# Kernel optimization log

Hardware: AMD Instinct MI355X
Metric: run time of the kernel (lower is better)

## Reference

```python
import jax, jax.numpy as jnp
import numpy as np

D_MODEL = 768
NUM_HEADS = 12
D_K = D_MODEL // NUM_HEADS


def setup_inputs() -> dict:
    key = jax.random.key(0)
    ks = jax.random.split(key, 12)
    B, S = 4, 2048
    s = 1.0 / np.sqrt(D_MODEL)
    inp = {
        "query": jax.random.normal(ks[0], (B, S, D_MODEL), jnp.float32),
        "key": jax.random.normal(ks[1], (B, S, D_MODEL), jnp.float32),
        "value": jax.random.normal(ks[2], (B, S, D_MODEL), jnp.float32),
        "Wq": jax.random.normal(ks[3], (D_MODEL, D_MODEL), jnp.float32) * s,
        "bq": jnp.zeros((D_MODEL,), jnp.float32),
        "Wk": jax.random.normal(ks[4], (D_MODEL, D_MODEL), jnp.float32) * s,
        "bk": jnp.zeros((D_MODEL,), jnp.float32),
        "Wv": jax.random.normal(ks[5], (D_MODEL, D_MODEL), jnp.float32) * s,
        "bv": jnp.zeros((D_MODEL,), jnp.float32),
        "Wo": jax.random.normal(ks[6], (D_MODEL, D_MODEL), jnp.float32) * s,
        "bo": jnp.zeros((D_MODEL,), jnp.float32),
    }
    return inp


def _split_heads(x):
    B, S, _ = x.shape
    return x.reshape(B, S, NUM_HEADS, D_K).transpose(0, 2, 1, 3)  # [B,H,S,Dk]


def reference(query, key, value, Wq, bq, Wk, bk, Wv, bv, Wo, bo):
    # Linear projections (torch nn.Linear: x @ W.T + b)
    Q = _split_heads(query @ Wq.T + bq)
    K = _split_heads(key @ Wk.T + bk)
    V = _split_heads(value @ Wv.T + bv)
    scale = 1.0 / jnp.sqrt(jnp.asarray(D_K, Q.dtype))
    scores = jnp.einsum("bhqd,bhkd->bhqk", Q, K) * scale  # [B,H,S,S]
    attn = jax.nn.softmax(scores, axis=-1)
    # dropout is identity in eval mode
    out = jnp.einsum("bhqk,bhkd->bhqd", attn, V)  # [B,H,S,Dk]
    B, H, S, Dk = out.shape
    out = out.transpose(0, 2, 1, 3).reshape(B, S, H * Dk)
    return out @ Wo.T + bo
```

## Files before the change

kernel.cpp:

```cpp
#include <hip/hip_runtime.h>
#include <hip/hip_bf16.h>

typedef _Float16 half8 __attribute__((ext_vector_type(8)));
typedef _Float16 h4 __attribute__((ext_vector_type(4)));
typedef __fp16 fp16x2 __attribute__((ext_vector_type(2)));
typedef float f32x4 __attribute__((ext_vector_type(4)));

#define D_MODEL 768
#define NUM_HEADS 12
#define D_K 64
#define SEQ 2048
#define BATCH 4
#define M_TOTAL (BATCH * SEQ)
#define W_ELEMS (D_MODEL * D_MODEL)
#define X_ELEMS (M_TOTAL * D_MODEL)
#define QSCALE 0.18033688011112042f
#define SOFF 4.0f

__device__ __forceinline__ void gll16(const _Float16* g, _Float16* l) {
    __builtin_amdgcn_global_load_lds(
        (const __attribute__((address_space(1))) unsigned int*)g,
        (__attribute__((address_space(3))) unsigned int*)l,
        16, 0, 0);
}

__global__ void convert_all(
    const float* __restrict__ w0, const float* __restrict__ w1,
    const float* __restrict__ w2, const float* __restrict__ w3,
    const float* __restrict__ x0, const float* __restrict__ x1,
    const float* __restrict__ x2, _Float16* __restrict__ dst)
{
    const size_t W4 = W_ELEMS / 4, X4 = X_ELEMS / 4;
    size_t i = (size_t)blockIdx.x * blockDim.x + threadIdx.x;
    const float* src;
    size_t off;
    if (i < 4 * W4) {
        size_t slab = i / W4;
        off = i - slab * W4;
        src = (slab == 0) ? w0 : (slab == 1) ? w1 : (slab == 2) ? w2 : w3;
    } else {
        size_t j = i - 4 * W4;
        size_t slab = j / X4;
        off = j - slab * X4;
        src = (slab == 0) ? x0 : (slab == 1) ? x1 : x2;
    }
    float4 f = ((const float4*)src)[off];
    h4 h;
    h[0] = (_Float16)f.x; h[1] = (_Float16)f.y;
    h[2] = (_Float16)f.z; h[3] = (_Float16)f.w;
    ((h4*)dst)[i] = h;
}

__global__ __launch_bounds__(256) void gemm_qkv(
    const _Float16* __restrict__ Xall, const _Float16* __restrict__ Wall,
    const float* __restrict__ bq, const float* __restrict__ bk, const float* __restrict__ bv,
    _Float16* __restrict__ Qo, _Float16* __restrict__ Ko, _Float16* __restrict__ Vto)
{
    __shared__ __align__(16) char smem[36864];
    _Float16* As = (_Float16*)smem;
    _Float16* Bs = As + 128 * 64;

    const int z = blockIdx.z;
    const _Float16* X = Xall + (size_t)z * X_ELEMS;
    const _Float16* W = Wall + (size_t)z * W_ELEMS;

    const int t = threadIdx.x;
    const int w = t >> 6;
    const int l = t & 63;
    const int ln = t & 15;
    const int quad = (t >> 4) & 3;
    const int wm = w >> 1, wn = w & 1;
    const int m0 = blockIdx.x * 128, n0 = blockIdx.y * 128;

    const int srow = l >> 3;
    const int scol = (l & 7) ^ srow;

    f32x4 acc[4][4] = {};

    for (int k0 = 0; k0 < D_MODEL; k0 += 64) {
#pragma unroll
        for (int jj = 0; jj < 4; ++jj) {
            int j = w * 4 + jj;
            int row = j * 8 + srow;
            gll16(X + (size_t)(m0 + row) * D_MODEL + k0 + scol * 8, As + j * 512);
            gll16(W + (size_t)(n0 + row) * D_MODEL + k0 + scol * 8, Bs + j * 512);
        }
        __syncthreads();

#pragma unroll
        for (int kk = 0; kk < 2; ++kk) {
            half8 a[4], b[4];
#pragma unroll
            for (int i = 0; i < 4; ++i) {
                int ra = wm * 64 + i * 16 + ln;
                int rb = wn * 64 + i * 16 + ln;
                a[i] = *(const half8*)&As[ra * 64 + (((kk * 4 + quad) ^ (ln & 7)) * 8)];
                b[i] = *(const half8*)&Bs[rb * 64 + (((kk * 4 + quad) ^ (ln & 7)) * 8)];
            }
            if (z <= 1) {
#pragma unroll
                for (int i = 0; i < 4; ++i)
#pragma unroll
                    for (int j2 = 0; j2 < 4; ++j2)
                        acc[i][j2] = __builtin_amdgcn_mfma_f32_16x16x32_f16(b[j2], a[i], acc[i][j2], 0, 0, 0);
            } else {
#pragma unroll
                for (int i = 0; i < 4; ++i)
#pragma unroll
                    for (int j2 = 0; j2 < 4; ++j2)
                        acc[i][j2] = __builtin_amdgcn_mfma_f32_16x16x32_f16(a[i], b[j2], acc[i][j2], 0, 0, 0);
            }
        }
        __syncthreads();
    }

    if (z <= 1) {
        const float* bias = (z == 0) ? bq : bk;
        _Float16* dst = (z == 0) ? Qo : Ko;
        const int head = (n0 + wn * 64) >> 6;
#pragma unroll
        for (int i = 0; i < 4; ++i) {
            int m = m0 + wm * 64 + i * 16 + ln;
            int b_ = m >> 11, s_ = m & 2047;
            _Float16* rowp = dst + ((size_t)((b_ * NUM_HEADS + head) * SEQ + s_)) * D_K;
#pragma unroll
            for (int j = 0; j < 4; ++j) {
                int dbase = j * 16 + quad * 4;
                f32x4 bn = *(const f32x4*)&bias[n0 + wn * 64 + dbase];
                h4 o;
#pragma unroll
                for (int r = 0; r < 4; ++r) {
                    float v = acc[i][j][r] + bn[r];
                    if (z == 0) v *= QSCALE;
                    o[r] = (_Float16)v;
                }
                *(h4*)&rowp[dbase] = o;
            }
        }
    } else {
        const float* bias = bv;
        _Float16* T = (_Float16*)smem + (size_t)w * (64 * 72);
#pragma unroll
        for (int i = 0; i < 4; ++i) {
#pragma unroll
            for (int j = 0; j < 4; ++j) {
                float bn = bias[n0 + wn * 64 + j * 16 + ln];
                h4 hh;
#pragma unroll
                for (int r = 0; r < 4; ++r) hh[r] = (_Float16)(acc[i][j][r] + bn);
                *(h4*)&T[(j * 16 + ln) * 72 + i * 16 + quad * 4] = hh;
            }
        }
        const int b_ = m0 >> 11;
        const int s0 = (m0 & 2047) + wm * 64;
        const int head = (n0 >> 6) + wn;
        _Float16* base = Vto + (size_t)(b_ * NUM_HEADS + head) * D_K * SEQ + s0;
        const int p = l & 7, tt = p >> 2, qq = p & 3;
#pragma unroll
        for (int r8 = 0; r8 < 8; ++r8) {
            int nl = r8 * 8 + (l >> 3);
            h4 lo = *(const h4*)&T[nl * 72 + tt * 32 + qq * 4];
            h4 hi = *(const h4*)&T[nl * 72 + tt * 32 + 16 + qq * 4];
            half8 v = __builtin_shufflevector(lo, hi, 0, 1, 2, 3, 4, 5, 6, 7);
            *(half8*)(base + (size_t)nl * SEQ + p * 8) = v;
        }
    }
}

__global__ __launch_bounds__(512, 6) void attn(
    const _Float16* __restrict__ Qg, const _Float16* __restrict__ Kg,
    const _Float16* __restrict__ Vtg, _Float16* __restrict__ ctx)
{
    __shared__ __align__(16) _Float16 Ks[2][64 * 64];
    __shared__ __align__(16) _Float16 Vs[2][64 * 64];

    const int t = threadIdx.x;
    const int w = t >> 6;
    const int l = t & 63;
    const int ln = t & 15;
    const int quad = (t >> 4) & 3;

    const int lid = blockIdx.x + (int)gridDim.x * blockIdx.y;
    const int nid = (lid & 7) * ((SEQ / 128) * (BATCH * NUM_HEADS) / 8) + (lid >> 3);
    const int bh = nid >> 4;
    const int q0 = (nid & 15) * 128 + w * 16;

    const _Float16* Qh = Qg + (size_t)bh * SEQ * D_K;
    const _Float16* Kh = Kg + (size_t)bh * SEQ * D_K;
    const _Float16* Vh = Vtg + (size_t)bh * D_K * SEQ;

    const int srow = l >> 3;
    const int scol = (l & 7) ^ srow;
    const _Float16* Ksrc = Kh + (size_t)(w * 8 + srow) * D_K + scol * 8;
    const _Float16* Vsrc = Vh + (size_t)(w * 8 + srow) * SEQ + scol * 8;

    half8 qf[2];
#pragma unroll
    for (int dh = 0; dh < 2; ++dh)
        qf[dh] = *(const half8*)(Qh + (size_t)(q0 + ln) * D_K + dh * 32 + quad * 8);

    f32x4 acc[4] = {};
    f32x4 lsum = {};

    gll16(Ksrc, &Ks[0][w * 512]);
    gll16(Vsrc, &Vs[0][w * 512]);
    asm volatile("s_waitcnt vmcnt(0)" ::: "memory");
    __builtin_amdgcn_s_barrier();

    int cur = 0;
    for (int c = 0; c < SEQ / 64; ++c) {
        if (c + 1 < SEQ / 64) {
            gll16(Ksrc + (size_t)(c + 1) * 64 * D_K, &Ks[cur ^ 1][w * 512]);
            gll16(Vsrc + (size_t)(c + 1) * 64, &Vs[cur ^ 1][w * 512]);
        }

        const _Float16* Ksc = Ks[cur];
        const _Float16* Vsc = Vs[cur];

        h4 pB[4];
#pragma unroll
        for (int kt = 0; kt < 4; ++kt) {
            half8 kf0 = *(const half8*)&Ksc[(kt * 16 + ln) * 64 + ((quad ^ (ln & 7)) * 8)];
            half8 kf1 = *(const half8*)&Ksc[(kt * 16 + ln) * 64 + (((4 + quad) ^ (ln & 7)) * 8)];
            f32x4 s = {-SOFF, -SOFF, -SOFF, -SOFF};
            s = __builtin_amdgcn_mfma_f32_16x16x32_f16(kf0, qf[0], s, 0, 0, 0);
            s = __builtin_amdgcn_mfma_f32_16x16x32_f16(kf1, qf[1], s, 0, 0, 0);
            f32x4 p;
            p[0] = __builtin_amdgcn_exp2f(s[0]);
            p[1] = __builtin_amdgcn_exp2f(s[1]);
            p[2] = __builtin_amdgcn_exp2f(s[2]);
            p[3] = __builtin_amdgcn_exp2f(s[3]);
            lsum += p;
            fp16x2 r0 = __builtin_amdgcn_cvt_pkrtz(p[0], p[1]);
            fp16x2 r1 = __builtin_amdgcn_cvt_pkrtz(p[2], p[3]);
            h4 h;
            h[0] = (_Float16)r0[0]; h[1] = (_Float16)r0[1];
            h[2] = (_Float16)r1[0]; h[3] = (_Float16)r1[1];
            pB[kt] = h;
        }

        half8 pB80 = __builtin_shufflevector(pB[0], pB[1], 0, 1, 2, 3, 4, 5, 6, 7);
        half8 pB81 = __builtin_shufflevector(pB[2], pB[3], 0, 1, 2, 3, 4, 5, 6, 7);

        __builtin_amdgcn_s_setprio(1);
#pragma unroll
        for (int dt = 0; dt < 4; ++dt) {
            const int row = (dt * 16 + ln) * 64;
            half8 va = *(const half8*)&Vsc[row + ((quad ^ (ln & 7)) * 8)];
            half8 vb = *(const half8*)&Vsc[row + (((4 + quad) ^ (ln & 7)) * 8)];
            acc[dt] = __builtin_amdgcn_mfma_f32_16x16x32_f16(va, pB80, acc[dt], 0, 0, 0);
            acc[dt] = __builtin_amdgcn_mfma_f32_16x16x32_f16(vb, pB81, acc[dt], 0, 0, 0);
        }
        __builtin_amdgcn_s_setprio(0);

        asm volatile("s_waitcnt vmcnt(0)" ::: "memory");
        __builtin_amdgcn_s_barrier();
        cur ^= 1;
    }

    const int h = bh % NUM_HEADS, b = bh / NUM_HEADS;
    {
        float lp = lsum[0] + lsum[1] + lsum[2] + lsum[3];
        lp += __shfl_xor(lp, 16);
        lp += __shfl_xor(lp, 32);
        float rinv = __builtin_amdgcn_rcpf(lp);
        int q = q0 + ln;
#pragma unroll
        for (int dt = 0; dt < 4; ++dt) {
            h4 o;
            o[0] = (_Float16)(acc[dt][0] * rinv);
            o[1] = (_Float16)(acc[dt][1] * rinv);
            o[2] = (_Float16)(acc[dt][2] * rinv);
            o[3] = (_Float16)(acc[dt][3] * rinv);
            *(h4*)&ctx[((size_t)(b * SEQ + q)) * D_MODEL + h * D_K + dt * 16 + quad * 4] = o;
        }
    }
}

__global__ __launch_bounds__(256) void gemm_out(
    const _Float16* __restrict__ A, const _Float16* __restrict__ W,
    const float* __restrict__ bo, float* __restrict__ out)
{
    __shared__ __align__(16) _Float16 As[128 * 64];
    __shared__ __align__(16) _Float16 Bs[128 * 64];

    const int t = threadIdx.x;
    const int w = t >> 6;
    const int l = t & 63;
    const int ln = t & 15;
    const int quad = (t >> 4) & 3;
    const int wm = w >> 1, wn = w & 1;
    const int m0 = blockIdx.x * 128, n0 = blockIdx.y * 128;

    const int srow = l >> 3;
    const int scol = (l & 7) ^ srow;

    f32x4 acc[4][4] = {};

    for (int k0 = 0; k0 < D_MODEL; k0 += 64) {
#pragma unroll
        for (int jj = 0; jj < 4; ++jj) {
            int j = w * 4 + jj;
            int row = j * 8 + srow;
            gll16(A + (size_t)(m0 + row) * D_MODEL + k0 + scol * 8, As + j * 512);
            gll16(W + (size_t)(n0 + row) * D_MODEL + k0 + scol * 8, Bs + j * 512);
        }
        __syncthreads();

#pragma unroll
        for (int kk = 0; kk < 2; ++kk) {
            half8 a[4], b[4];
#pragma unroll
            for (int i = 0; i < 4; ++i) {
                int ra = wm * 64 + i * 16 + ln;
                int rb = wn * 64 + i * 16 + ln;
                a[i] = *(const half8*)&As[ra * 64 + (((kk * 4 + quad) ^ (ln & 7)) * 8)];
                b[i] = *(const half8*)&Bs[rb * 64 + (((kk * 4 + quad) ^ (ln & 7)) * 8)];
            }
#pragma unroll
            for (int i = 0; i < 4; ++i)
#pragma unroll
                for (int j2 = 0; j2 < 4; ++j2)
                    acc[i][j2] = __builtin_amdgcn_mfma_f32_16x16x32_f16(b[j2], a[i], acc[i][j2], 0, 0, 0);
        }
        __syncthreads();
    }

#pragma unroll
    for (int i = 0; i < 4; ++i) {
        int m = m0 + wm * 64 + i * 16 + ln;
        float* rowp = out + (size_t)m * D_MODEL;
#pragma unroll
        for (int j = 0; j < 4; ++j) {
            int nb = n0 + wn * 64 + j * 16 + quad * 4;
            f32x4 o = acc[i][j] + *(const f32x4*)&bo[nb];
            *(f32x4*)&rowp[nb] = o;
        }
    }
}

extern "C" void kernel_launch(void* const* d_in, const int* in_sizes, int n_in,
                              void* d_out, int out_size, void* d_ws, size_t ws_size,
                              hipStream_t stream) {
    const float* query = (const float*)d_in[0];
    const float* key   = (const float*)d_in[1];
    const float* value = (const float*)d_in[2];
    const float* Wq = (const float*)d_in[3];
    const float* bq = (const float*)d_in[4];
    const float* Wk = (const float*)d_in[5];
    const float* bk = (const float*)d_in[6];
    const float* Wv = (const float*)d_in[7];
    const float* bv = (const float*)d_in[8];
    const float* Wo = (const float*)d_in[9];
    const float* bo = (const float*)d_in[10];
    float* out = (float*)d_out;

    _Float16* ws = (_Float16*)d_ws;
    _Float16* Wb  = ws;
    _Float16* Xb  = Wb + 4 * (size_t)W_ELEMS;
    _Float16* Qb  = Xb + 3 * (size_t)X_ELEMS;
    _Float16* Kb  = Qb + (size_t)X_ELEMS;
    _Float16* Vtb = Kb + (size_t)X_ELEMS;
    _Float16* ctx = Vtb + (size_t)X_ELEMS;

    const size_t total4 = (4 * (size_t)W_ELEMS + 3 * (size_t)X_ELEMS) / 4;
    convert_all<<<(int)(total4 / 256), 256, 0, stream>>>(
        Wq, Wk, Wv, Wo, query, key, value, Wb);

    gemm_qkv<<<dim3(M_TOTAL / 128, D_MODEL / 128, 3), 256, 0, stream>>>(
        Xb, Wb, bq, bk, bv, Qb, Kb, Vtb);

    attn<<<dim3(SEQ / 128, BATCH * NUM_HEADS), 512, 0, stream>>>(Qb, Kb, Vtb, ctx);

    gemm_out<<<dim3(M_TOTAL / 128, D_MODEL / 128), 256, 0, stream>>>(
        ctx, Wb + 3 * (size_t)W_ELEMS, bo, out);
}
```

Baseline: 258.6 us.

## Shrink attention blocks to 64 queries and halve V-transpose LDS staging

The attention kernel now uses 256-thread blocks that each cover 64 queries, and every wave loads two K/V rows per tile so the 64-row tiles are still filled. Launch bounds change from (512,6) to (256,5), and the swizzled LDS row offsets are hoisted out of the inner loop. In the QKV GEMM, the V transpose epilogue now stages in two halves through a 64x36 buffer instead of 64x72, which cuts static LDS from 36 KB to 32 KB to allow more resident blocks. The trade-off is that each K/V tile is reused by fewer query rows, so twice as many blocks reload the same K/V data.

```diff
diff --git a/kernel.cpp b/kernel.cpp
--- a/kernel.cpp
+++ b/kernel.cpp
@@ -56,7 +56,7 @@
     const float* __restrict__ bq, const float* __restrict__ bk, const float* __restrict__ bv,
     _Float16* __restrict__ Qo, _Float16* __restrict__ Ko, _Float16* __restrict__ Vto)
 {
-    __shared__ __align__(16) char smem[36864];
+    __shared__ __align__(16) char smem[32768];
     _Float16* As = (_Float16*)smem;
     _Float16* Bs = As + 128 * 64;
 
@@ -139,35 +139,39 @@
         }
     } else {
         const float* bias = bv;
-        _Float16* T = (_Float16*)smem + (size_t)w * (64 * 72);
-#pragma unroll
-        for (int i = 0; i < 4; ++i) {
-#pragma unroll
-            for (int j = 0; j < 4; ++j) {
-                float bn = bias[n0 + wn * 64 + j * 16 + ln];
-                h4 hh;
-#pragma unroll
-                for (int r = 0; r < 4; ++r) hh[r] = (_Float16)(acc[i][j][r] + bn);
-                *(h4*)&T[(j * 16 + ln) * 72 + i * 16 + quad * 4] = hh;
-            }
-        }
+        _Float16* T = (_Float16*)smem + (size_t)w * (64 * 36);
         const int b_ = m0 >> 11;
         const int s0 = (m0 & 2047) + wm * 64;
         const int head = (n0 >> 6) + wn;
         _Float16* base = Vto + (size_t)(b_ * NUM_HEADS + head) * D_K * SEQ + s0;
-        const int p = l & 7, tt = p >> 2, qq = p & 3;
-#pragma unroll
-        for (int r8 = 0; r8 < 8; ++r8) {
-            int nl = r8 * 8 + (l >> 3);
-            h4 lo = *(const h4*)&T[nl * 72 + tt * 32 + qq * 4];
-            h4 hi = *(const h4*)&T[nl * 72 + tt * 32 + 16 + qq * 4];
-            half8 v = __builtin_shufflevector(lo, hi, 0, 1, 2, 3, 4, 5, 6, 7);
-            *(half8*)(base + (size_t)nl * SEQ + p * 8) = v;
-        }
-    }
-}
-
-__global__ __launch_bounds__(512, 6) void attn(
+        const int qq = l & 3;
+#pragma unroll
+        for (int half = 0; half < 2; ++half) {
+#pragma unroll
+            for (int i2 = 0; i2 < 2; ++i2) {
+                int i = half * 2 + i2;
+#pragma unroll
+                for (int j = 0; j < 4; ++j) {
+                    float bn = bias[n0 + wn * 64 + j * 16 + ln];
+                    h4 hh;
+#pragma unroll
+                    for (int r = 0; r < 4; ++r) hh[r] = (_Float16)(acc[i][j][r] + bn);
+                    *(h4*)&T[(j * 16 + ln) * 36 + i2 * 16 + quad * 4] = hh;
+                }
+            }
+#pragma unroll
+            for (int r4 = 0; r4 < 4; ++r4) {
+                int nl = r4 * 16 + (l >> 2);
+                h4 lo = *(const h4*)&T[nl * 36 + qq * 4];
+                h4 hi = *(const h4*)&T[nl * 36 + 16 + qq * 4];
+                half8 v = __builtin_shufflevector(lo, hi, 0, 1, 2, 3, 4, 5, 6, 7);
+                *(half8*)(base + (size_t)nl * SEQ + (half * 4 + qq) * 8) = v;
+            }
+        }
+    }
+}
+
+__global__ __launch_bounds__(256, 5) void attn(
     const _Float16* __restrict__ Qg, const _Float16* __restrict__ Kg,
     const _Float16* __restrict__ Vtg, _Float16* __restrict__ ctx)
 {
@@ -181,9 +185,9 @@
     const int quad = (t >> 4) & 3;
 
     const int lid = blockIdx.x + (int)gridDim.x * blockIdx.y;
-    const int nid = (lid & 7) * ((SEQ / 128) * (BATCH * NUM_HEADS) / 8) + (lid >> 3);
-    const int bh = nid >> 4;
-    const int q0 = (nid & 15) * 128 + w * 16;
+    const int nid = (lid & 7) * ((SEQ / 64) * (BATCH * NUM_HEADS) / 8) + (lid >> 3);
+    const int bh = nid >> 5;
+    const int q0 = (nid & 31) * 64 + w * 16;
 
     const _Float16* Qh = Qg + (size_t)bh * SEQ * D_K;
     const _Float16* Kh = Kg + (size_t)bh * SEQ * D_K;
@@ -191,27 +195,41 @@
 
     const int srow = l >> 3;
     const int scol = (l & 7) ^ srow;
-    const _Float16* Ksrc = Kh + (size_t)(w * 8 + srow) * D_K + scol * 8;
-    const _Float16* Vsrc = Vh + (size_t)(w * 8 + srow) * SEQ + scol * 8;
+    const _Float16* Ksrc0 = Kh + (size_t)(w * 16 + srow) * D_K + scol * 8;
+    const _Float16* Ksrc1 = Kh + (size_t)(w * 16 + 8 + srow) * D_K + scol * 8;
+    const _Float16* Vsrc0 = Vh + (size_t)(w * 16 + srow) * SEQ + scol * 8;
+    const _Float16* Vsrc1 = Vh + (size_t)(w * 16 + 8 + srow) * SEQ + scol * 8;
 
     half8 qf[2];
 #pragma unroll
     for (int dh = 0; dh < 2; ++dh)
         qf[dh] = *(const half8*)(Qh + (size_t)(q0 + ln) * D_K + dh * 32 + quad * 8);
 
+    int roff[4];
+#pragma unroll
+    for (int x = 0; x < 4; ++x) roff[x] = (x * 16 + ln) * 64;
+    const int c0 = (quad ^ (ln & 7)) * 8;
+    const int c1 = ((4 + quad) ^ (ln & 7)) * 8;
+
     f32x4 acc[4] = {};
     f32x4 lsum = {};
 
-    gll16(Ksrc, &Ks[0][w * 512]);
-    gll16(Vsrc, &Vs[0][w * 512]);
+    gll16(Ksrc0, &Ks[0][w * 1024]);
+    gll16(Ksrc1, &Ks[0][w * 1024 + 512]);
+    gll16(Vsrc0, &Vs[0][w * 1024]);
+    gll16(Vsrc1, &Vs[0][w * 1024 + 512]);
     asm volatile("s_waitcnt vmcnt(0)" ::: "memory");
     __builtin_amdgcn_s_barrier();
 
     int cur = 0;
     for (int c = 0; c < SEQ / 64; ++c) {
         if (c + 1 < SEQ / 64) {
-            gll16(Ksrc + (size_t)(c + 1) * 64 * D_K, &Ks[cur ^ 1][w * 512]);
-            gll16(Vsrc + (size_t)(c + 1) * 64, &Vs[cur ^ 1][w * 512]);
+            const size_t koff = (size_t)(c + 1) * 64 * D_K;
+            const size_t voff = (size_t)(c + 1) * 64;
+            gll16(Ksrc0 + koff, &Ks[cur ^ 1][w * 1024]);
+            gll16(Ksrc1 + koff, &Ks[cur ^ 1][w * 1024 + 512]);
+            gll16(Vsrc0 + voff, &Vs[cur ^ 1][w * 1024]);
+            gll16(Vsrc1 + voff, &Vs[cur ^ 1][w * 1024 + 512]);
         }
 
         const _Float16* Ksc = Ks[cur];
@@ -220,8 +238,8 @@
         h4 pB[4];
 #pragma unroll
         for (int kt = 0; kt < 4; ++kt) {
-            half8 kf0 = *(const half8*)&Ksc[(kt * 16 + ln) * 64 + ((quad ^ (ln & 7)) * 8)];
-            half8 kf1 = *(const half8*)&Ksc[(kt * 16 + ln) * 64 + (((4 + quad) ^ (ln & 7)) * 8)];
+            half8 kf0 = *(const half8*)&Ksc[roff[kt] + c0];
+            half8 kf1 = *(const half8*)&Ksc[roff[kt] + c1];
             f32x4 s = {-SOFF, -SOFF, -SOFF, -SOFF};
             s = __builtin_amdgcn_mfma_f32_16x16x32_f16(kf0, qf[0], s, 0, 0, 0);
             s = __builtin_amdgcn_mfma_f32_16x16x32_f16(kf1, qf[1], s, 0, 0, 0);
@@ -245,9 +263,8 @@
         __builtin_amdgcn_s_setprio(1);
 #pragma unroll
         for (int dt = 0; dt < 4; ++dt) {
-            const int row = (dt * 16 + ln) * 64;
-            half8 va = *(const half8*)&Vsc[row + ((quad ^ (ln & 7)) * 8)];
-            half8 vb = *(const half8*)&Vsc[row + (((4 + quad) ^ (ln & 7)) * 8)];
+            half8 va = *(const half8*)&Vsc[roff[dt] + c0];
+            half8 vb = *(const half8*)&Vsc[roff[dt] + c1];
             acc[dt] = __builtin_amdgcn_mfma_f32_16x16x32_f16(va, pB80, acc[dt], 0, 0, 0);
             acc[dt] = __builtin_amdgcn_mfma_f32_16x16x32_f16(vb, pB81, acc[dt], 0, 0, 0);
         }
@@ -370,7 +387,7 @@
     gemm_qkv<<<dim3(M_TOTAL / 128, D_MODEL / 128, 3), 256, 0, stream>>>(
         Xb, Wb, bq, bk, bv, Qb, Kb, Vtb);
 
-    attn<<<dim3(SEQ / 128, BATCH * NUM_HEADS), 512, 0, stream>>>(Qb, Kb, Vtb, ctx);
+    attn<<<dim3(SEQ / 64, BATCH * NUM_HEADS), 256, 0, stream>>>(Qb, Kb, Vtb, ctx);
 
     gemm_out<<<dim3(M_TOTAL / 128, D_MODEL / 128), 256, 0, stream>>>(
         ctx, Wb + 3 * (size_t)W_ELEMS, bo, out);
```

Measured after the change: 276.2 us. 1.07x slower.

## Triple-buffer K/V tiles in attention loop with partial vmcnt waits

Applied to the files above, without the earlier changes.

Converts the attention kernel's double-buffered K/V LDS staging into a three-stage ring. Loads are issued two chunks ahead, and each step waits with vmcnt(2) so the newest prefetch can stay in flight. This is meant to hide global-to-LDS load latency better and cut the full drain before every barrier. In exchange, LDS per block grows from 32KB to 48KB, which may reduce the number of resident blocks per CU.

```diff
diff --git a/kernel.cpp b/kernel.cpp
--- a/kernel.cpp
+++ b/kernel.cpp
@@ -171,8 +171,8 @@
     const _Float16* __restrict__ Qg, const _Float16* __restrict__ Kg,
     const _Float16* __restrict__ Vtg, _Float16* __restrict__ ctx)
 {
-    __shared__ __align__(16) _Float16 Ks[2][64 * 64];
-    __shared__ __align__(16) _Float16 Vs[2][64 * 64];
+    __shared__ __align__(16) _Float16 Ks[3][64 * 64];
+    __shared__ __align__(16) _Float16 Vs[3][64 * 64];
 
     const int t = threadIdx.x;
     const int w = t >> 6;
@@ -202,26 +202,23 @@
     f32x4 acc[4] = {};
     f32x4 lsum = {};
 
-    gll16(Ksrc, &Ks[0][w * 512]);
-    gll16(Vsrc, &Vs[0][w * 512]);
-    asm volatile("s_waitcnt vmcnt(0)" ::: "memory");
-    __builtin_amdgcn_s_barrier();
-
-    int cur = 0;
-    for (int c = 0; c < SEQ / 64; ++c) {
-        if (c + 1 < SEQ / 64) {
-            gll16(Ksrc + (size_t)(c + 1) * 64 * D_K, &Ks[cur ^ 1][w * 512]);
-            gll16(Vsrc + (size_t)(c + 1) * 64, &Vs[cur ^ 1][w * 512]);
-        }
-
-        const _Float16* Ksc = Ks[cur];
-        const _Float16* Vsc = Vs[cur];
+    const int c0 = (quad ^ (ln & 7)) * 8;
+    const int c1 = ((4 + quad) ^ (ln & 7)) * 8;
+
+    auto stage = [&](int c, int B) {
+        gll16(Ksrc + (size_t)c * 64 * D_K, &Ks[B][w * 512]);
+        gll16(Vsrc + (size_t)c * 64, &Vs[B][w * 512]);
+    };
+
+    auto compute = [&](int B) {
+        const _Float16* Ksc = Ks[B];
+        const _Float16* Vsc = Vs[B];
 
         h4 pB[4];
 #pragma unroll
         for (int kt = 0; kt < 4; ++kt) {
-            half8 kf0 = *(const half8*)&Ksc[(kt * 16 + ln) * 64 + ((quad ^ (ln & 7)) * 8)];
-            half8 kf1 = *(const half8*)&Ksc[(kt * 16 + ln) * 64 + (((4 + quad) ^ (ln & 7)) * 8)];
+            half8 kf0 = *(const half8*)&Ksc[(kt * 16 + ln) * 64 + c0];
+            half8 kf1 = *(const half8*)&Ksc[(kt * 16 + ln) * 64 + c1];
             f32x4 s = {-SOFF, -SOFF, -SOFF, -SOFF};
             s = __builtin_amdgcn_mfma_f32_16x16x32_f16(kf0, qf[0], s, 0, 0, 0);
             s = __builtin_amdgcn_mfma_f32_16x16x32_f16(kf1, qf[1], s, 0, 0, 0);
@@ -245,18 +242,39 @@
         __builtin_amdgcn_s_setprio(1);
 #pragma unroll
         for (int dt = 0; dt < 4; ++dt) {
-            const int row = (dt * 16 + ln) * 64;
-            half8 va = *(const half8*)&Vsc[row + ((quad ^ (ln & 7)) * 8)];
-            half8 vb = *(const half8*)&Vsc[row + (((4 + quad) ^ (ln & 7)) * 8)];
+            half8 va = *(const half8*)&Vsc[(dt * 16 + ln) * 64 + c0];
+            half8 vb = *(const half8*)&Vsc[(dt * 16 + ln) * 64 + c1];
             acc[dt] = __builtin_amdgcn_mfma_f32_16x16x32_f16(va, pB80, acc[dt], 0, 0, 0);
             acc[dt] = __builtin_amdgcn_mfma_f32_16x16x32_f16(vb, pB81, acc[dt], 0, 0, 0);
         }
         __builtin_amdgcn_s_setprio(0);
-
-        asm volatile("s_waitcnt vmcnt(0)" ::: "memory");
+    };
+
+    stage(0, 0);
+    stage(1, 1);
+
+    for (int c = 0; c < 30; c += 3) {
+        asm volatile("s_waitcnt vmcnt(2)" ::: "memory");
         __builtin_amdgcn_s_barrier();
-        cur ^= 1;
-    }
+        stage(c + 2, 2);
+        compute(0);
+
+        asm volatile("s_waitcnt vmcnt(2)" ::: "memory");
+        __builtin_amdgcn_s_barrier();
+        stage(c + 3, 0);
+        compute(1);
+
+        asm volatile("s_waitcnt vmcnt(2)" ::: "memory");
+        __builtin_amdgcn_s_barrier();
+        stage(c + 4, 1);
+        compute(2);
+    }
+    asm volatile("s_waitcnt vmcnt(2)" ::: "memory");
+    __builtin_amdgcn_s_barrier();
+    compute(0);
+    asm volatile("s_waitcnt vmcnt(0)" ::: "memory");
+    __builtin_amdgcn_s_barrier();
+    compute(1);
 
     const int h = bh % NUM_HEADS, b = bh / NUM_HEADS;
     {
```

New measurement: 257.7 us. No clear change (-0.4%).
